# Performance work log

Hardware: AMD Instinct MI355X
Metric: run time of the kernel (lower is better)

## Reference

```python
import jax, jax.numpy as jnp
import numpy as np

H = 16  # num_heads

def setup_inputs() -> dict:
    key = jax.random.key(0)
    k1, k2, k3 = jax.random.split(key, 3)
    D = 1024
    x = jax.random.normal(k1, (4, 2048, D), dtype=jnp.float32)
    W_qkv = jax.random.normal(k2, (D, 3 * D), dtype=jnp.float32) * (1.0 / np.sqrt(D))
    b_qkv = jnp.zeros((3 * D,), dtype=jnp.float32)
    W_out = jax.random.normal(k3, (D, D), dtype=jnp.float32) * (1.0 / np.sqrt(D))
    b_out = jnp.zeros((D,), dtype=jnp.float32)
    return {"x": x, "W_qkv": W_qkv, "b_qkv": b_qkv, "W_out": W_out, "b_out": b_out}

def reference(x, W_qkv, b_qkv, W_out, b_out):
    B, S, D = x.shape
    hd = D // H  # head_dim
    qkv = x @ W_qkv + b_qkv  # [B,S,3D]
    q, k, v = jnp.split(qkv, 3, axis=-1)
    # [B,S,D] -> [B,H,S,hd]
    q = q.reshape(B, S, H, hd).transpose(0, 2, 1, 3)
    k = k.reshape(B, S, H, hd).transpose(0, 2, 1, 3)
    v = v.reshape(B, S, H, hd).transpose(0, 2, 1, 3)
    scores = jnp.einsum('bhqd,bhkd->bhqk', q, k) / jnp.sqrt(jnp.float32(hd))
    weights = jax.nn.softmax(scores, axis=-1)  # dropout p=0.0 (eval)
    out = jnp.einsum('bhqk,bhkd->bhqd', weights, v)
    out = out.transpose(0, 2, 1, 3).reshape(B, S, D)
    return out @ W_out + b_out
```

## Files before the change

kernel.cpp:

```cpp
#include <hip/hip_runtime.h>

typedef __bf16 bf16;
typedef __bf16 bf16x4 __attribute__((ext_vector_type(4)));
typedef __bf16 bf16x8 __attribute__((ext_vector_type(8)));
typedef float f32x4 __attribute__((ext_vector_type(4)));
typedef unsigned u32x2 __attribute__((ext_vector_type(2)));

static constexpr int NB = 4;
static constexpr int NS = 2048;
static constexpr int ND = 1024;
static constexpr int NH = 16;
static constexpr int HD = 64;
static constexpr float QSCALE = 0.18033688011112042f;

#define GL16(g, l)                                                             \
    __builtin_amdgcn_global_load_lds(                                          \
        (const __attribute__((address_space(1))) void*)(g),                    \
        (__attribute__((address_space(3))) void*)(l), 16, 0, 0)

static __device__ __forceinline__ unsigned pk2(float a, float b) {
    union { __bf16 h[2]; unsigned u; } t;
    t.h[0] = (__bf16)a; t.h[1] = (__bf16)b;
    return t.u;
}

__global__ void k_conv(const float* __restrict__ in, bf16* __restrict__ out, int n) {
    int i = (blockIdx.x * blockDim.x + threadIdx.x) * 4;
    if (i < n) {
        float4 v = *reinterpret_cast<const float4*>(in + i);
        bf16* o = out + i;
        o[0] = (bf16)v.x; o[1] = (bf16)v.y; o[2] = (bf16)v.z; o[3] = (bf16)v.w;
    }
}

__global__ void k_transconv(const float* __restrict__ in, bf16* __restrict__ out,
                            int K, int N) {
    __shared__ float tile[32][33];
    int k0 = blockIdx.y * 32, n0 = blockIdx.x * 32;
    int tx = threadIdx.x, ty = threadIdx.y;
    for (int j = 0; j < 32; j += 8)
        tile[ty + j][tx] = in[(long)(k0 + ty + j) * N + n0 + tx];
    __syncthreads();
    for (int j = 0; j < 32; j += 8)
        out[(long)(n0 + ty + j) * K + k0 + tx] = (bf16)tile[tx][ty + j];
}

template <int MODE>
__global__ __launch_bounds__(256, 2) void k_gemm(
    const bf16* __restrict__ A, const bf16* __restrict__ Bt,
    const float* __restrict__ bias,
    void* __restrict__ out0, void* __restrict__ out1,
    int M, int Kd)
{
    constexpr int BM = 128, BN = 128, BK = 64;
    __shared__ __align__(16) bf16 As[2][BM * BK];
    __shared__ __align__(16) bf16 Bs[2][BN * BK];

    const int t = threadIdx.x;
    const int wid = t >> 6, lane = t & 63;
    const int wm = wid >> 1, wn = wid & 1;
    const int m0 = blockIdx.y * BM, n0 = blockIdx.x * BN;
    const int lrow = lane & 15, lhi = lane >> 4;

    const int srow0 = wid * 32 + (lane >> 3);
    const int scol = ((lane & 7) ^ (lane >> 3)) * 8;
    const bf16* ag = A + (long)(m0 + srow0) * Kd + scol;
    const bf16* bg = Bt + (long)(n0 + srow0) * Kd + scol;

    auto STAGE = [&](int buf_, int k0_) {
#pragma unroll
        for (int c = 0; c < 4; ++c) {
            GL16(ag + (long)(c * 8) * Kd + k0_, &As[buf_][(wid * 32 + c * 8) * BK]);
            GL16(bg + (long)(c * 8) * Kd + k0_, &Bs[buf_][(wid * 32 + c * 8) * BK]);
        }
    };

    f32x4 acc[4][4] = {};
    const int nt = Kd >> 6;
    const int swzr = (lrow & 7) << 4;
    int co[2];
#pragma unroll
    for (int kk = 0; kk < 2; ++kk)
        co[kk] = ((kk * 64 + lhi * 16) ^ swzr) >> 1;

    STAGE(0, 0);
    int cur = 0;
    for (int tix = 0; tix < nt; ++tix) {
        if (tix + 1 < nt) {
            STAGE(cur ^ 1, (tix + 1) * BK);
            asm volatile("s_waitcnt vmcnt(8)" ::: "memory");
        } else {
            asm volatile("s_waitcnt vmcnt(0)" ::: "memory");
        }
        __builtin_amdgcn_s_barrier();
        __builtin_amdgcn_sched_barrier(0);

        bf16x8 af[2][4], bfr[2][4];
#pragma unroll
        for (int kk = 0; kk < 2; ++kk)
#pragma unroll
            for (int i = 0; i < 4; ++i) {
                af[kk][i]  = *reinterpret_cast<const bf16x8*>(
                    &As[cur][(wm * 64 + i * 16 + lrow) * BK + co[kk]]);
                bfr[kk][i] = *reinterpret_cast<const bf16x8*>(
                    &Bs[cur][(wn * 64 + i * 16 + lrow) * BK + co[kk]]);
            }
        __builtin_amdgcn_s_setprio(1);
#pragma unroll
        for (int kk = 0; kk < 2; ++kk)
#pragma unroll
            for (int i = 0; i < 4; ++i)
#pragma unroll
                for (int j = 0; j < 4; ++j) {
                    if (MODE == 1)
                        acc[i][j] = __builtin_amdgcn_mfma_f32_16x16x32_bf16(
                            af[kk][i], bfr[kk][j], acc[i][j], 0, 0, 0);
                    else
                        acc[i][j] = __builtin_amdgcn_mfma_f32_16x16x32_bf16(
                            bfr[kk][j], af[kk][i], acc[i][j], 0, 0, 0);
                }
        __builtin_amdgcn_s_setprio(0);
        __builtin_amdgcn_s_barrier();
        cur ^= 1;
    }

    const int colbase = n0 + wn * 64;

    if (MODE == 0) {
        bf16* eb = (bf16*)As + wid * 4096;
        const bool isQ = (colbase >> 10) == 0;
#pragma unroll
        for (int j = 0; j < 4; ++j) {
            f32x4 bv = *reinterpret_cast<const f32x4*>(&bias[colbase + j * 16 + 4 * lhi]);
#pragma unroll
            for (int i = 0; i < 4; ++i) {
                int srt = i * 16 + lrow;
                bf16x4 pk;
#pragma unroll
                for (int r = 0; r < 4; ++r) {
                    float v = acc[i][j][r] + bv[r];
                    pk[r] = (bf16)(isQ ? v * QSCALE : v);
                }
                *reinterpret_cast<bf16x4*>(
                    reinterpret_cast<char*>(eb) + srt * 128 +
                    (((j * 16 + 4 * lhi) * 2) ^ ((srt & 7) << 4))) = pk;
            }
        }
        const int h = (colbase & 1023) >> 6;
        bf16* Ob = isQ ? (bf16*)out0 : (bf16*)out1;
#pragma unroll
        for (int it = 0; it < 8; ++it) {
            int rt = it * 8 + (lane >> 3);
            bf16x8 v = *reinterpret_cast<const bf16x8*>(
                reinterpret_cast<char*>(eb) + rt * 128 +
                (((lane & 7) * 16) ^ ((rt & 7) << 4)));
            int row = m0 + wm * 64 + rt;
            int bb = row >> 11, s = row & 2047;
            long bh = (long)bb * NH + h;
            *reinterpret_cast<bf16x8*>(&Ob[(bh * NS + s) * HD + (lane & 7) * 8]) = v;
        }
    } else if (MODE == 1) {
        bf16* eb = (bf16*)As + wid * 4096;
#pragma unroll
        for (int j = 0; j < 4; ++j) {
            float bv = bias[colbase + j * 16 + lrow];
            int drt = j * 16 + lrow;
#pragma unroll
            for (int i = 0; i < 4; ++i) {
                bf16x4 pk;
#pragma unroll
                for (int r = 0; r < 4; ++r) pk[r] = (bf16)(acc[i][j][r] + bv);
                *reinterpret_cast<bf16x4*>(
                    reinterpret_cast<char*>(eb) + drt * 128 +
                    (((i * 16 + 4 * lhi) * 2) ^ ((drt & 7) << 4))) = pk;
            }
        }
        const int h = (colbase & 1023) >> 6;
        const int mrow = m0 + wm * 64;
        const int bb = mrow >> 11, s0 = mrow & 2047;
        bf16* Vt = (bf16*)out0;
#pragma unroll
        for (int it = 0; it < 8; ++it) {
            int dt = it * 8 + (lane >> 3);
            bf16x8 v = *reinterpret_cast<const bf16x8*>(
                reinterpret_cast<char*>(eb) + dt * 128 +
                (((lane & 7) * 16) ^ ((dt & 7) << 4)));
            long bh = (long)bb * NH + h;
            *reinterpret_cast<bf16x8*>(&Vt[(bh * HD + dt) * NS + s0 + (lane & 7) * 8]) = v;
        }
    } else {
        float* ef = (float*)As + wid * 2048;
        float* O = (float*)out0;
#pragma unroll
        for (int half = 0; half < 2; ++half) {
#pragma unroll
            for (int i2 = 0; i2 < 2; ++i2) {
                int i = half * 2 + i2;
                int srt = i2 * 16 + lrow;
#pragma unroll
                for (int j = 0; j < 4; ++j) {
                    f32x4 bv = *reinterpret_cast<const f32x4*>(
                        &bias[colbase + j * 16 + 4 * lhi]);
                    f32x4 v = acc[i][j] + bv;
                    *reinterpret_cast<f32x4*>(
                        reinterpret_cast<char*>(ef) + srt * 256 +
                        (((j * 16 + 4 * lhi) * 4) ^ ((srt & 7) << 4))) = v;
                }
            }
#pragma unroll
            for (int it = 0; it < 8; ++it) {
                int rt = it * 4 + (lane >> 4);
                f32x4 v = *reinterpret_cast<const f32x4*>(
                    reinterpret_cast<char*>(ef) + rt * 256 +
                    (((lane & 15) * 16) ^ ((rt & 7) << 4)));
                int row = m0 + wm * 64 + half * 32 + rt;
                *reinterpret_cast<f32x4*>(
                    &O[(long)row * 1024 + colbase + (lane & 15) * 4]) = v;
            }
            asm volatile("" ::: "memory");
        }
    }
}

__global__ __launch_bounds__(256, 4) void k_attn(
    const bf16* __restrict__ Qb, const bf16* __restrict__ Kb,
    const bf16* __restrict__ Vt, bf16* __restrict__ Ao)
{
    constexpr int KB = 64;
    constexpr int NT = NS / KB;
    __shared__ __align__(16) bf16 Ks[2][KB * HD];
    __shared__ __align__(16) bf16 Vs[2][HD * KB];
    __shared__ __align__(16) bf16 Ps[4 * 16 * 64];

    const int t = threadIdx.x;
    const int wid = t >> 6, lane = t & 63;
    const int lrow = lane & 15, lhi = lane >> 4;

    const int flat = blockIdx.y * gridDim.x + blockIdx.x;
    const int n = (flat & 7) * 128 + (flat >> 3);
    const int bh = n >> 4;
    const int qw = (n & 15) * 128 + wid * 32;

    const bf16* Qg = Qb + ((long)bh * NS + qw) * HD;
    const bf16* Kg = Kb + (long)bh * NS * HD;
    const bf16* Vg = Vt + (long)bh * HD * NS;

    bf16x8 qf[2][2];
#pragma unroll
    for (int qfr = 0; qfr < 2; ++qfr)
#pragma unroll
        for (int c = 0; c < 2; ++c)
            qf[qfr][c] = *reinterpret_cast<const bf16x8*>(
                Qg + (long)(qfr * 16 + lrow) * HD + c * 32 + lhi * 8);

    f32x4 of[2][4] = {};
    float lsum[2] = {0.f, 0.f};

    const int gsr = lane >> 3;
    const int gsc = ((lane & 7) ^ gsr) * 8;
    auto STAGE = [&](int buf, int kb) {
#pragma unroll
        for (int c = 0; c < 2; ++c) {
            const int rb = wid * 16 + c * 8;
            GL16(Kg + (long)(kb + rb + gsr) * HD + gsc, &Ks[buf][rb * 64]);
            GL16(Vg + (long)(rb + gsr) * NS + kb + gsc, &Vs[buf][rb * 64]);
        }
    };

    const int rsw = (lrow & 7) << 4;
    bf16* psw = &Ps[wid * 1024 + lrow * 64];

    auto COMPUTE = [&](int b_) {
        f32x4 st[2][4] = {};
        __builtin_amdgcn_s_setprio(1);
#pragma unroll
        for (int j = 0; j < 4; ++j)
#pragma unroll
            for (int c = 0; c < 2; ++c) {
                bf16x8 kf = *reinterpret_cast<const bf16x8*>(
                    &Ks[b_][(j * 16 + lrow) * 64 + (((c * 64 + lhi * 16) ^ rsw) >> 1)]);
#pragma unroll
                for (int qfr = 0; qfr < 2; ++qfr)
                    st[qfr][j] = __builtin_amdgcn_mfma_f32_16x16x32_bf16(
                        kf, qf[qfr][c], st[qfr][j], 0, 0, 0);
            }
        __builtin_amdgcn_s_setprio(0);

        bf16x8 pfr[2][2];
#pragma unroll
        for (int qfr = 0; qfr < 2; ++qfr) {
#pragma unroll
            for (int j = 0; j < 4; ++j) {
                float e0 = __builtin_amdgcn_exp2f(st[qfr][j][0]);
                float e1 = __builtin_amdgcn_exp2f(st[qfr][j][1]);
                float e2 = __builtin_amdgcn_exp2f(st[qfr][j][2]);
                float e3 = __builtin_amdgcn_exp2f(st[qfr][j][3]);
                lsum[qfr] += (e0 + e1) + (e2 + e3);
                u32x2 w; w[0] = pk2(e0, e1); w[1] = pk2(e2, e3);
                *reinterpret_cast<u32x2*>(
                    reinterpret_cast<char*>(psw) + (((j * 32 + lhi * 8) ^ rsw))) = w;
            }
            asm volatile("" ::: "memory");
#pragma unroll
            for (int chunk = 0; chunk < 2; ++chunk)
                pfr[qfr][chunk] = *reinterpret_cast<const bf16x8*>(
                    reinterpret_cast<char*>(psw) + ((chunk * 64 + lhi * 16) ^ rsw));
            asm volatile("" ::: "memory");
        }

        __builtin_amdgcn_s_setprio(1);
#pragma unroll
        for (int chunk = 0; chunk < 2; ++chunk)
#pragma unroll
            for (int f = 0; f < 4; ++f) {
                bf16x8 vf = *reinterpret_cast<const bf16x8*>(
                    &Vs[b_][(f * 16 + lrow) * 64 +
                            (((chunk * 64 + lhi * 16) ^ rsw) >> 1)]);
#pragma unroll
                for (int qfr = 0; qfr < 2; ++qfr)
                    of[qfr][f] = __builtin_amdgcn_mfma_f32_16x16x32_bf16(
                        vf, pfr[qfr][chunk], of[qfr][f], 0, 0, 0);
            }
        __builtin_amdgcn_s_setprio(0);
    };

    STAGE(0, 0);
    int cur = 0;
    for (int it = 0; it < NT; ++it) {
        if (it + 1 < NT) {
            STAGE(cur ^ 1, (it + 1) * KB);
            asm volatile("s_waitcnt vmcnt(4)" ::: "memory");
        } else {
            asm volatile("s_waitcnt vmcnt(0)" ::: "memory");
        }
        __builtin_amdgcn_s_barrier();
        __builtin_amdgcn_sched_barrier(0);
        COMPUTE(cur);
        __builtin_amdgcn_s_barrier();
        cur ^= 1;
    }

#pragma unroll
    for (int qfr = 0; qfr < 2; ++qfr) {
        lsum[qfr] += __shfl_xor(lsum[qfr], 16);
        lsum[qfr] += __shfl_xor(lsum[qfr], 32);
    }

    bf16* eb = (bf16*)Ks + wid * 2048;
#pragma unroll
    for (int qfr = 0; qfr < 2; ++qfr) {
        float inv = 1.0f / lsum[qfr];
        int srt = qfr * 16 + lrow;
#pragma unroll
        for (int f = 0; f < 4; ++f) {
            bf16x4 pk;
#pragma unroll
            for (int r = 0; r < 4; ++r) pk[r] = (bf16)(of[qfr][f][r] * inv);
            *reinterpret_cast<bf16x4*>(
                reinterpret_cast<char*>(eb) + srt * 128 +
                (((f * 16 + 4 * lhi) * 2) ^ ((srt & 7) << 4))) = pk;
        }
    }
    const int bb = bh >> 4, h = bh & 15;
#pragma unroll
    for (int it = 0; it < 4; ++it) {
        int rt = it * 8 + (lane >> 3);
        bf16x8 v = *reinterpret_cast<const bf16x8*>(
            reinterpret_cast<char*>(eb) + rt * 128 +
            (((lane & 7) * 16) ^ ((rt & 7) << 4)));
        int s = qw + rt;
        *reinterpret_cast<bf16x8*>(
            &Ao[((long)bb * NS + s) * ND + h * HD + (lane & 7) * 8]) = v;
    }
}

extern "C" void kernel_launch(void* const* d_in, const int* in_sizes, int n_in,
                              void* d_out, int out_size, void* d_ws, size_t ws_size,
                              hipStream_t stream) {
    const float* x    = (const float*)d_in[0];
    const float* Wqkv = (const float*)d_in[1];
    const float* bqkv = (const float*)d_in[2];
    const float* Wout = (const float*)d_in[3];
    const float* bout = (const float*)d_in[4];
    float* out = (float*)d_out;

    char* ws = (char*)d_ws;
    bf16* Xb  = (bf16*)(ws);
    bf16* Wqt = (bf16*)(ws + 16777216);
    bf16* Wot = (bf16*)(ws + 23068672);
    bf16* Qb  = (bf16*)(ws + 25165824);
    bf16* Kb  = (bf16*)(ws + 41943040);
    bf16* Vt  = (bf16*)(ws + 58720256);
    bf16* Ab  = (bf16*)(ws + 75497472);

    k_conv<<<dim3(8192), dim3(256), 0, stream>>>(x, Xb, NB * NS * ND);
    k_transconv<<<dim3(96, 32), dim3(32, 8), 0, stream>>>(Wqkv, Wqt, ND, 3 * ND);
    k_transconv<<<dim3(32, 32), dim3(32, 8), 0, stream>>>(Wout, Wot, ND, ND);

    k_gemm<0><<<dim3(16, 64), dim3(256), 0, stream>>>(
        Xb, Wqt, bqkv, Qb, Kb, NB * NS, ND);
    k_gemm<1><<<dim3(8, 64), dim3(256), 0, stream>>>(
        Xb, Wqt + (long)2048 * ND, bqkv + 2048, Vt, nullptr, NB * NS, ND);

    k_attn<<<dim3(16, 64), dim3(256), 0, stream>>>(Qb, Kb, Vt, Ab);

    k_gemm<2><<<dim3(8, 64), dim3(256), 0, stream>>>(
        Ab, Wot, bout, out, nullptr, NB * NS, ND);
}
```

Measured before the change: 199.3 us.

## Single-buffer attention K/V LDS via register prefetch to raise occupancy

Swaps the double-buffered direct global-to-LDS loads of K and V for a single LDS buffer. The next tile is prefetched into registers and written to LDS after a barrier. LDS per block shrinks from about 40KB to 24KB, so launch bounds go from 4 to 6 blocks per SM to hide latency with more waves. The cost is extra VGPRs for the prefetch, an extra LDS write pass, and full vmcnt(0) waits each iteration. The epilogue staging buffer is split across Ks and Vs to fit the smaller LDS.

```diff
diff --git a/kernel.cpp b/kernel.cpp
--- a/kernel.cpp
+++ b/kernel.cpp
@@ -222,14 +222,14 @@
     }
 }
 
-__global__ __launch_bounds__(256, 4) void k_attn(
+__global__ __launch_bounds__(256, 6) void k_attn(
     const bf16* __restrict__ Qb, const bf16* __restrict__ Kb,
     const bf16* __restrict__ Vt, bf16* __restrict__ Ao)
 {
     constexpr int KB = 64;
     constexpr int NT = NS / KB;
-    __shared__ __align__(16) bf16 Ks[2][KB * HD];
-    __shared__ __align__(16) bf16 Vs[2][HD * KB];
+    __shared__ __align__(16) bf16 Ks[KB * HD];
+    __shared__ __align__(16) bf16 Vs[HD * KB];
     __shared__ __align__(16) bf16 Ps[4 * 16 * 64];
 
     const int t = threadIdx.x;
@@ -258,19 +258,32 @@
 
     const int gsr = lane >> 3;
     const int gsc = ((lane & 7) ^ gsr) * 8;
-    auto STAGE = [&](int buf, int kb) {
+    bf16x8 sk[2], sv[2];
+    auto LOADREGS = [&](int kb) {
 #pragma unroll
         for (int c = 0; c < 2; ++c) {
             const int rb = wid * 16 + c * 8;
-            GL16(Kg + (long)(kb + rb + gsr) * HD + gsc, &Ks[buf][rb * 64]);
-            GL16(Vg + (long)(rb + gsr) * NS + kb + gsc, &Vs[buf][rb * 64]);
+            sk[c] = *reinterpret_cast<const bf16x8*>(
+                Kg + (long)(kb + rb + gsr) * HD + gsc);
+            sv[c] = *reinterpret_cast<const bf16x8*>(
+                Vg + (long)(rb + gsr) * NS + kb + gsc);
+        }
+    };
+    auto WRITELDS = [&]() {
+#pragma unroll
+        for (int c = 0; c < 2; ++c) {
+            const int rb = wid * 16 + c * 8;
+            *reinterpret_cast<bf16x8*>(
+                reinterpret_cast<char*>(&Ks[rb * 64]) + lane * 16) = sk[c];
+            *reinterpret_cast<bf16x8*>(
+                reinterpret_cast<char*>(&Vs[rb * 64]) + lane * 16) = sv[c];
         }
     };
 
     const int rsw = (lrow & 7) << 4;
     bf16* psw = &Ps[wid * 1024 + lrow * 64];
 
-    auto COMPUTE = [&](int b_) {
+    auto COMPUTE = [&]() {
         f32x4 st[2][4] = {};
         __builtin_amdgcn_s_setprio(1);
 #pragma unroll
@@ -278,7 +291,7 @@
 #pragma unroll
             for (int c = 0; c < 2; ++c) {
                 bf16x8 kf = *reinterpret_cast<const bf16x8*>(
-                    &Ks[b_][(j * 16 + lrow) * 64 + (((c * 64 + lhi * 16) ^ rsw) >> 1)]);
+                    &Ks[(j * 16 + lrow) * 64 + (((c * 64 + lhi * 16) ^ rsw) >> 1)]);
 #pragma unroll
                 for (int qfr = 0; qfr < 2; ++qfr)
                     st[qfr][j] = __builtin_amdgcn_mfma_f32_16x16x32_bf16(
@@ -314,8 +327,8 @@
 #pragma unroll
             for (int f = 0; f < 4; ++f) {
                 bf16x8 vf = *reinterpret_cast<const bf16x8*>(
-                    &Vs[b_][(f * 16 + lrow) * 64 +
-                            (((chunk * 64 + lhi * 16) ^ rsw) >> 1)]);
+                    &Vs[(f * 16 + lrow) * 64 +
+                        (((chunk * 64 + lhi * 16) ^ rsw) >> 1)]);
 #pragma unroll
                 for (int qfr = 0; qfr < 2; ++qfr)
                     of[qfr][f] = __builtin_amdgcn_mfma_f32_16x16x32_bf16(
@@ -324,21 +337,18 @@
         __builtin_amdgcn_s_setprio(0);
     };
 
-    STAGE(0, 0);
-    int cur = 0;
+    LOADREGS(0);
     for (int it = 0; it < NT; ++it) {
-        if (it + 1 < NT) {
-            STAGE(cur ^ 1, (it + 1) * KB);
-            asm volatile("s_waitcnt vmcnt(4)" ::: "memory");
-        } else {
-            asm volatile("s_waitcnt vmcnt(0)" ::: "memory");
-        }
+        asm volatile("s_waitcnt vmcnt(0)" ::: "memory");
+        __builtin_amdgcn_s_barrier();
+        WRITELDS();
+        if (it + 1 < NT) LOADREGS((it + 1) * KB);
+        asm volatile("s_waitcnt lgkmcnt(0)" ::: "memory");
         __builtin_amdgcn_s_barrier();
         __builtin_amdgcn_sched_barrier(0);
-        COMPUTE(cur);
-        __builtin_amdgcn_s_barrier();
-        cur ^= 1;
-    }
+        COMPUTE();
+    }
+    __builtin_amdgcn_s_barrier();
 
 #pragma unroll
     for (int qfr = 0; qfr < 2; ++qfr) {
@@ -346,7 +356,7 @@
         lsum[qfr] += __shfl_xor(lsum[qfr], 32);
     }
 
-    bf16* eb = (bf16*)Ks + wid * 2048;
+    bf16* eb = (wid < 2) ? ((bf16*)Ks + wid * 2048) : ((bf16*)Vs + (wid - 2) * 2048);
 #pragma unroll
     for (int qfr = 0; qfr < 2; ++qfr) {
         float inv = 1.0f / lsum[qfr];
```

Result: slower. 618.0 us (+210.0%).
